# Kernel tuning notes

Measured on AMD Instinct MI355X. Metric: run time of the kernel, lower is better.

Reference implementation:

```python
import jax, jax.numpy as jnp
import numpy as np

N_NODES = 12288
N_EDGES = 393216
LATENT = 128
EDGE_F = 4


def setup_inputs() -> dict:
    key = jax.random.key(0)
    k1, k2, k3, k4 = jax.random.split(key, 4)
    z = jax.random.normal(k1, (N_NODES, LATENT), dtype=jnp.float32)
    edge_index = jax.random.randint(k2, (2, N_EDGES), 0, N_NODES, dtype=jnp.int64)
    edge_attr = jax.random.normal(k3, (N_EDGES, EDGE_F), dtype=jnp.float32)
    W = jax.random.normal(k4, (1, 2 * LATENT), dtype=jnp.float32) * (1.0 / np.sqrt(2 * LATENT))
    b = jnp.zeros((1,), dtype=jnp.float32)
    return {"z": z, "edge_index": edge_index, "edge_attr": edge_attr, "W": W, "b": b}


def reference(z, edge_index, edge_attr, W, b):
    # z: [N, D], edge_index: [2, E], edge_attr: [E, F], W: [1, 2D], b: [1]
    num_nodes = z.shape[0]
    row, col = edge_index[0], edge_index[1]
    # gather node embeddings per edge and apply tiny linear: [E, 2D] @ [2D, 1]
    edge_features = jnp.concatenate([z[row], z[col]], axis=1)
    specified_edge_probs = (edge_features @ W.T + b)[:, 0]  # [E]
    # scatter edge probs into dense NxN (indexed assignment, like torch)
    full_edge_probs = jnp.zeros((num_nodes, num_nodes), dtype=z.dtype).at[row, col].set(specified_edge_probs)
    # to_dense_adj scatter-adds edge_attr -> [N, N, F]; sum(dim=3) commutes, so add summed attr
    adj = jnp.zeros((num_nodes, num_nodes), dtype=edge_attr.dtype).at[row, col].add(edge_attr.sum(axis=1))
    return adj + full_edge_probs
```

## Files before the change

kernel.cpp:

```cpp
#include <hip/hip_runtime.h>

#define N_NODES 12288
#define N_EDGES 393216
#define LATENT  128

#define E_BITS  19
#define E_MASK  ((1u << E_BITS) - 1u)

__device__ __forceinline__ unsigned int hash32(unsigned int key) {
    key ^= key >> 16; key *= 0x85ebca6bu;
    key ^= key >> 13; key *= 0xc2b2ae35u;
    key ^= key >> 16;
    return key;
}

__global__ void node_dots(const float* __restrict__ z, const float* __restrict__ W,
                          float* __restrict__ s1, float* __restrict__ s2) {
    int node = (int)((blockIdx.x * blockDim.x + threadIdx.x) >> 6);
    int lane = (int)(threadIdx.x & 63);
    if (node >= N_NODES) return;
    const float* zr = z + (size_t)node * LATENT;
    float a  = zr[lane];
    float bb = zr[lane + 64];
    float p1 = a * W[lane]       + bb * W[lane + 64];
    float p2 = a * W[lane + 128] + bb * W[lane + 192];
    #pragma unroll
    for (int off = 32; off > 0; off >>= 1) {
        p1 += __shfl_down(p1, off, 64);
        p2 += __shfl_down(p2, off, 64);
    }
    if (lane == 0) { s1[node] = p1; s2[node] = p2; }
}

__global__ void edge_pass(const int* __restrict__ ei, const float* __restrict__ ea,
                          unsigned long long* __restrict__ table, unsigned int tab_mask,
                          float* __restrict__ out) {
    int e = (int)(blockIdx.x * blockDim.x + threadIdx.x);
    if (e >= N_EDGES) return;
    unsigned int r = (unsigned int)ei[e];
    unsigned int c = (unsigned int)ei[e + N_EDGES];
    unsigned int key = r * (unsigned int)N_NODES + c;

    float4 a4 = ((const float4*)ea)[e];
    atomicAdd(&out[(size_t)key], a4.x + a4.y + a4.z + a4.w);

    unsigned long long packed = (((unsigned long long)(key + 1u)) << E_BITS) | (unsigned int)e;
    unsigned int h = hash32(key) & tab_mask;
    for (;;) {
        unsigned long long old = atomicCAS(&table[h], 0ull, packed);
        if (old == 0ull) break;
        if ((unsigned int)(old >> E_BITS) == key + 1u) {
            atomicMax(&table[h], packed);
            break;
        }
        h = (h + 1u) & tab_mask;
    }
}

__global__ void add_probs(const unsigned long long* __restrict__ table, unsigned int tab_n,
                          const float* __restrict__ s1, const float* __restrict__ s2,
                          const float* __restrict__ bptr, float* __restrict__ out) {
    unsigned int i = blockIdx.x * blockDim.x + threadIdx.x;
    if (i >= tab_n) return;
    unsigned long long entry = table[i];
    if (entry == 0ull) return;
    unsigned int key = (unsigned int)(entry >> E_BITS) - 1u;
    unsigned int r = key / (unsigned int)N_NODES;
    unsigned int c = key - r * (unsigned int)N_NODES;
    out[(size_t)key] += s1[r] + s2[c] + bptr[0];
}

extern "C" void kernel_launch(void* const* d_in, const int* in_sizes, int n_in,
                              void* d_out, int out_size, void* d_ws, size_t ws_size,
                              hipStream_t stream) {
    const float* z  = (const float*)d_in[0];
    const int*   ei = (const int*)d_in[1];
    const float* ea = (const float*)d_in[2];
    const float* W  = (const float*)d_in[3];
    const float* b  = (const float*)d_in[4];
    float* out = (float*)d_out;

    char* ws = (char*)d_ws;
    float* s1 = (float*)ws;
    float* s2 = (float*)(ws + (size_t)N_NODES * sizeof(float));
    unsigned long long* table = (unsigned long long*)(ws + 2ull * N_NODES * sizeof(float));
    size_t head = 2ull * N_NODES * sizeof(float);

    int bits = (head + (8ull << 20) <= ws_size) ? 20 : 19;
    unsigned int tab_n = 1u << bits;
    unsigned int tab_mask = tab_n - 1u;
    size_t tab_bytes = 8ull << bits;

    hipMemsetAsync(d_out, 0, (size_t)out_size * sizeof(float), stream);
    hipMemsetAsync(table, 0, tab_bytes, stream);

    node_dots<<<N_NODES / 4, 256, 0, stream>>>(z, W, s1, s2);
    edge_pass<<<N_EDGES / 256, 256, 0, stream>>>(ei, ea, table, tab_mask, out);
    add_probs<<<tab_n / 256, 256, 0, stream>>>(table, tab_n, s1, s2, b, out);
}
```

Before: 683.7 us.

## Replace global hash table with row-bucketed CSR and per-row shared-memory hash

Edges are bucketed by source row through a histogram, a scan and a scatter. One block per row then dedups columns in a shared-memory hash, adding the edge probability once per unique (row, col). The same block zeroes its output row and writes the values, which removes the full-output memset, the global atomics on the dense output, and the large global hash table with its memset. In exchange it adds several small kernels, including a single-block scan. It also changes duplicate handling: the probability is added once regardless of which edge wins. The shared table holds 512 slots, so a row with more unique columns than that would loop forever.

```diff
diff --git a/kernel.cpp b/kernel.cpp
--- a/kernel.cpp
+++ b/kernel.cpp
@@ -3,16 +3,8 @@
 #define N_NODES 12288
 #define N_EDGES 393216
 #define LATENT  128
+#define SLOTS   512
 
-#define E_BITS  19
-#define E_MASK  ((1u << E_BITS) - 1u)
-
-__device__ __forceinline__ unsigned int hash32(unsigned int key) {
-    key ^= key >> 16; key *= 0x85ebca6bu;
-    key ^= key >> 13; key *= 0xc2b2ae35u;
-    key ^= key >> 16;
-    return key;
-}
 
 __global__ void node_dots(const float* __restrict__ z, const float* __restrict__ W,
                           float* __restrict__ s1, float* __restrict__ s2) {
@@ -32,42 +24,91 @@
     if (lane == 0) { s1[node] = p1; s2[node] = p2; }
 }
 
-__global__ void edge_pass(const int* __restrict__ ei, const float* __restrict__ ea,
-                          unsigned long long* __restrict__ table, unsigned int tab_mask,
-                          float* __restrict__ out) {
+__global__ void hist_rows(const int* __restrict__ ei, unsigned int* __restrict__ cnt) {
+    int e = (int)(blockIdx.x * blockDim.x + threadIdx.x);
+    if (e < N_EDGES) atomicAdd(&cnt[(unsigned int)ei[e]], 1u);
+}
+
+__global__ __launch_bounds__(1024) void scan_rows(const unsigned int* __restrict__ cnt,
+                                                  unsigned int* __restrict__ offs,
+                                                  unsigned int* __restrict__ cursor) {
+    __shared__ unsigned int part[1024];
+    int t = (int)threadIdx.x;
+    unsigned int local[12];
+    unsigned int s = 0;
+    #pragma unroll
+    for (int i = 0; i < 12; i++) { local[i] = s; s += cnt[t * 12 + i]; }
+    part[t] = s;
+    __syncthreads();
+    for (int off = 1; off < 1024; off <<= 1) {
+        unsigned int v = (t >= off) ? part[t - off] : 0u;
+        __syncthreads();
+        part[t] += v;
+        __syncthreads();
+    }
+    unsigned int base = (t > 0) ? part[t - 1] : 0u;
+    #pragma unroll
+    for (int i = 0; i < 12; i++) {
+        unsigned int o = base + local[i];
+        offs[t * 12 + i] = o;
+        cursor[t * 12 + i] = o;
+    }
+    if (t == 1023) offs[12288] = part[1023];
+}
+
+__global__ void bucket_scatter(const int* __restrict__ ei, const float* __restrict__ ea,
+                               unsigned int* __restrict__ cursor,
+                               unsigned int* __restrict__ bcol, float* __restrict__ bsum) {
     int e = (int)(blockIdx.x * blockDim.x + threadIdx.x);
     if (e >= N_EDGES) return;
     unsigned int r = (unsigned int)ei[e];
     unsigned int c = (unsigned int)ei[e + N_EDGES];
-    unsigned int key = r * (unsigned int)N_NODES + c;
-
     float4 a4 = ((const float4*)ea)[e];
-    atomicAdd(&out[(size_t)key], a4.x + a4.y + a4.z + a4.w);
-
-    unsigned long long packed = (((unsigned long long)(key + 1u)) << E_BITS) | (unsigned int)e;
-    unsigned int h = hash32(key) & tab_mask;
-    for (;;) {
-        unsigned long long old = atomicCAS(&table[h], 0ull, packed);
-        if (old == 0ull) break;
-        if ((unsigned int)(old >> E_BITS) == key + 1u) {
-            atomicMax(&table[h], packed);
-            break;
-        }
-        h = (h + 1u) & tab_mask;
-    }
+    unsigned int pos = atomicAdd(&cursor[r], 1u);
+    bcol[pos] = c;
+    bsum[pos] = a4.x + a4.y + a4.z + a4.w;
 }
 
-__global__ void add_probs(const unsigned long long* __restrict__ table, unsigned int tab_n,
-                          const float* __restrict__ s1, const float* __restrict__ s2,
-                          const float* __restrict__ bptr, float* __restrict__ out) {
-    unsigned int i = blockIdx.x * blockDim.x + threadIdx.x;
-    if (i >= tab_n) return;
-    unsigned long long entry = table[i];
-    if (entry == 0ull) return;
-    unsigned int key = (unsigned int)(entry >> E_BITS) - 1u;
-    unsigned int r = key / (unsigned int)N_NODES;
-    unsigned int c = key - r * (unsigned int)N_NODES;
-    out[(size_t)key] += s1[r] + s2[c] + bptr[0];
+__global__ __launch_bounds__(256) void row_fill(const unsigned int* __restrict__ offs,
+                                                const unsigned int* __restrict__ bcol,
+                                                const float* __restrict__ bsum,
+                                                const float* __restrict__ s1,
+                                                const float* __restrict__ s2,
+                                                const float* __restrict__ bptr,
+                                                float* __restrict__ out) {
+    __shared__ unsigned int hcol[SLOTS];
+    __shared__ float        hval[SLOTS];
+    int r = (int)blockIdx.x;
+    int t = (int)threadIdx.x;
+    for (int i = t; i < SLOTS; i += 256) { hcol[i] = 0u; hval[i] = 0.f; }
+    __syncthreads();
+
+    unsigned int beg = offs[r], end = offs[r + 1];
+    for (unsigned int i = beg + (unsigned int)t; i < end; i += 256u) {
+        unsigned int c = bcol[i];
+        float v = bsum[i];
+        unsigned int h = (c * 2654435761u) >> (32 - 9);
+        for (;;) {
+            unsigned int prev = atomicCAS(&hcol[h], 0u, c + 1u);
+            if (prev == 0u) {
+                v += s1[r] + s2[c] + bptr[0];
+                atomicAdd(&hval[h], v);
+                break;
+            }
+            if (prev == c + 1u) { atomicAdd(&hval[h], v); break; }
+            h = (h + 1u) & (SLOTS - 1u);
+        }
+    }
+    __syncthreads();
+
+    float4* out4 = (float4*)(out + (size_t)r * N_NODES);
+    float4 z = make_float4(0.f, 0.f, 0.f, 0.f);
+    #pragma unroll
+    for (int i = 0; i < 12; i++) out4[t + i * 256] = z;
+    __syncthreads();
+
+    for (int i = t; i < SLOTS; i += 256)
+        if (hcol[i]) out[(size_t)r * N_NODES + (size_t)(hcol[i] - 1u)] = hval[i];
 }
 
 extern "C" void kernel_launch(void* const* d_in, const int* in_sizes, int n_in,
@@ -81,20 +122,19 @@
     float* out = (float*)d_out;
 
     char* ws = (char*)d_ws;
-    float* s1 = (float*)ws;
-    float* s2 = (float*)(ws + (size_t)N_NODES * sizeof(float));
-    unsigned long long* table = (unsigned long long*)(ws + 2ull * N_NODES * sizeof(float));
-    size_t head = 2ull * N_NODES * sizeof(float);
+    float*        s1     = (float*)(ws + 0);
+    float*        s2     = (float*)(ws + 49152);
+    unsigned int* cnt    = (unsigned int*)(ws + 98304);
+    unsigned int* offs   = (unsigned int*)(ws + 147456);
+    unsigned int* cursor = (unsigned int*)(ws + 197632);
+    unsigned int* bcol   = (unsigned int*)(ws + 246784);
+    float*        bsum   = (float*)(ws + 1819648);
 
-    int bits = (head + (8ull << 20) <= ws_size) ? 20 : 19;
-    unsigned int tab_n = 1u << bits;
-    unsigned int tab_mask = tab_n - 1u;
-    size_t tab_bytes = 8ull << bits;
-
-    hipMemsetAsync(d_out, 0, (size_t)out_size * sizeof(float), stream);
-    hipMemsetAsync(table, 0, tab_bytes, stream);
+    hipMemsetAsync(cnt, 0, N_NODES * sizeof(unsigned int), stream);
 
     node_dots<<<N_NODES / 4, 256, 0, stream>>>(z, W, s1, s2);
-    edge_pass<<<N_EDGES / 256, 256, 0, stream>>>(ei, ea, table, tab_mask, out);
-    add_probs<<<tab_n / 256, 256, 0, stream>>>(table, tab_n, s1, s2, b, out);
+    hist_rows<<<N_EDGES / 256, 256, 0, stream>>>(ei, cnt);
+    scan_rows<<<1, 1024, 0, stream>>>(cnt, offs, cursor);
+    bucket_scatter<<<N_EDGES / 256, 256, 0, stream>>>(ei, ea, cursor, bcol, bsum);
+    row_fill<<<N_NODES, 256, 0, stream>>>(offs, bcol, bsum, s1, s2, b, out);
 }
```

Result: faster. 665.8 us (-2.6%).
